# Performance work log

Measured on AMD Instinct MI355X. Metric: run time of the kernel, lower is better.

Reference implementation:

```python
import jax, jax.numpy as jnp
import numpy as np


def setup_inputs() -> dict:
    key = jax.random.key(0)
    ks = jax.random.split(key, 6)
    B, L, F, C, H, D1 = 262144, 20, 7, 16, 16, 8
    s = 0.1
    return {
        "x": jax.random.normal(ks[0], (B, L, F), dtype=jnp.float32),
        "conv_w": jax.random.normal(ks[1], (3, F, C), dtype=jnp.float32) * s,
        "conv_b": jnp.zeros((C,), dtype=jnp.float32),
        "rnn_w": jax.random.normal(ks[2], (C, H), dtype=jnp.float32) * s,
        "rnn_u": jax.random.normal(ks[3], (H, H), dtype=jnp.float32) * s,
        "rnn_b": jnp.zeros((H,), dtype=jnp.float32),
        "d1_w": jax.random.normal(ks[4], (H, D1), dtype=jnp.float32) * s,
        "d1_b": jnp.zeros((D1,), dtype=jnp.float32),
        "out_w": jax.random.normal(ks[5], (D1, 1), dtype=jnp.float32) * s,
        "out_b": jnp.zeros((1,), dtype=jnp.float32),
    }


def reference(x, conv_w, conv_b, rnn_w, rnn_u, rnn_b, d1_w, d1_b, out_w, out_b):
    # Conv1D, kernel 3, 'same' padding, relu.  x: [B,L,F] -> [B,L,C]
    h = jax.lax.conv_general_dilated(
        x, conv_w, window_strides=(1,), padding="SAME",
        dimension_numbers=("NWC", "WIO", "NWC"))
    h = jax.nn.relu(h + conv_b)

    # SimpleRNN(16), tanh, return last state.  Precompute input projections.
    xw = jnp.einsum("blc,ch->blh", h, rnn_w) + rnn_b  # [B,L,H]
    xw_t = jnp.swapaxes(xw, 0, 1)                      # [L,B,H]

    def step(state, xt):
        new = jnp.tanh(xt + state @ rnn_u)
        return new, None

    h0 = jnp.zeros((x.shape[0], rnn_u.shape[0]), dtype=x.dtype)
    h_last, _ = jax.lax.scan(step, h0, xw_t)           # [B,H]

    z = jax.nn.relu(h_last @ d1_w + d1_b)              # [B,8]
    return z @ out_w + out_b                           # [B,1]
```

## Files before the change

kernel.cpp:

```cpp
#include <hip/hip_runtime.h>


#define BLK 256
#define LSEQ 20
#define EPD 92
#define LOG2E2 2.8853900817779268f

typedef _Float16 f16;
typedef __fp16   fp16x2 __attribute__((ext_vector_type(2)));
typedef _Float16 f16x4 __attribute__((ext_vector_type(4)));
typedef _Float16 f16x8 __attribute__((ext_vector_type(8)));
typedef float    f32x4 __attribute__((ext_vector_type(4)));

union UB128 { uint4 q; f16x8 v; };
union UB64  { f16x4 v; fp16x2 p[2]; };
union HU    { fp16x2 p; uint u; };

__global__ __launch_bounds__(BLK, 6) void hybrid_fwd(
    const float* __restrict__ x,
    const float* __restrict__ conv_w, const float* __restrict__ conv_b,
    const float* __restrict__ rnn_w,  const float* __restrict__ rnn_u,
    const float* __restrict__ rnn_b,
    const float* __restrict__ d1_w,   const float* __restrict__ d1_b,
    const float* __restrict__ out_w,  const float* __restrict__ out_b,
    float* __restrict__ out)
{
    __shared__ __align__(16) uint xs[64 * EPD];

    const int tid  = threadIdx.x;
    const int wave = tid >> 6, lane = tid & 63;
    const int b16  = lane & 15, g = lane >> 4;
    const long BE  = (long)blockIdx.x * 64;

    #pragma unroll
    for (int k = 0; k < 3; ++k) {
        int t = tid + k * BLK;
        int e = t / 12, s = t - e * 12;
        xs[e * EPD + (s < 4 ? s : 80 + s)] = ((s & 3) == 3) ? 0x3C000000u : 0u;
    }
    const float* xg = x + BE * 140;
    #pragma unroll 2
    for (int k = 0; k < 5; ++k) {
        int t = tid + k * BLK;
        int e = t / 20, r = t - e * 20;
        const float* rp = xg + e * 140 + r * 7;
        float f0 = rp[0], f1 = rp[1], f2 = rp[2], f3 = rp[3];
        float f4 = rp[4], f5 = rp[5], f6 = rp[6];
        HU h0, h1, h2, h3;
        h0.p = __builtin_amdgcn_cvt_pkrtz(f0, f1);
        h1.p = __builtin_amdgcn_cvt_pkrtz(f2, f3);
        h2.p = __builtin_amdgcn_cvt_pkrtz(f4, f5);
        h3.p = __builtin_amdgcn_cvt_pkrtz(f6, 1.0f);
        uint4 val; val.x = h0.u; val.y = h1.u; val.z = h2.u; val.w = h3.u;
        *(uint4*)&xs[e * EPD + 4 * (r + 1)] = val;
    }
    __syncthreads();

    f16x8 A1;
    #pragma unroll
    for (int t = 0; t < 8; ++t) {
        float wv = conv_w[min(g * 7 + t, 20) * 16 + b16];
        float sel = (g < 3 && t < 7) ? wv
                  : ((g == 3 && t == 7) ? conv_b[b16] : 0.f);
        A1[t] = (f16)sel;
    }
    f16x4 A2, AU;
    f32x4 rbp;
    #pragma unroll
    for (int t = 0; t < 4; ++t) {
        A2[t]  = (f16)(LOG2E2 * rnn_w[(4 * g + t) * 16 + b16]);
        AU[t]  = (f16)(LOG2E2 * rnn_u[(4 * g + t) * 16 + b16]);
        rbp[t] = LOG2E2 * rnn_b[4 * g + t];
    }
    const f32x4 zero4 = {0.f, 0.f, 0.f, 0.f};

    const uint* rbase = xs + (wave * 16 + b16) * EPD + 4 * g;

    f16x4 H = {};

    #pragma unroll 4
    for (int l = 0; l < LSEQ; ++l) {
        UB128 B1;
        B1.q = *(const uint4*)(rbase + 4 * l);
        f32x4 a1 = __builtin_amdgcn_mfma_f32_16x16x32_f16(A1, B1.v, zero4, 0, 0, 0);
        UB64 B2;
        B2.p[0] = __builtin_amdgcn_cvt_pkrtz(fmaxf(a1[0], 0.f), fmaxf(a1[1], 0.f));
        B2.p[1] = __builtin_amdgcn_cvt_pkrtz(fmaxf(a1[2], 0.f), fmaxf(a1[3], 0.f));
        f32x4 a2 = __builtin_amdgcn_mfma_f32_16x16x16f16(A2, B2.v, rbp, 0, 0, 0);
        a2 = __builtin_amdgcn_mfma_f32_16x16x16f16(AU, H, a2, 0, 0, 0);
        float t0 = __builtin_amdgcn_rcpf(1.f + __builtin_amdgcn_exp2f(a2[0]));
        float t1 = __builtin_amdgcn_rcpf(1.f + __builtin_amdgcn_exp2f(a2[1]));
        float t2 = __builtin_amdgcn_rcpf(1.f + __builtin_amdgcn_exp2f(a2[2]));
        float t3 = __builtin_amdgcn_rcpf(1.f + __builtin_amdgcn_exp2f(a2[3]));
        UB64 Hn;
        Hn.p[0] = __builtin_amdgcn_cvt_pkrtz(fmaf(-2.f, t0, 1.f), fmaf(-2.f, t1, 1.f));
        Hn.p[1] = __builtin_amdgcn_cvt_pkrtz(fmaf(-2.f, t2, 1.f), fmaf(-2.f, t3, 1.f));
        H = Hn.v;
    }

    f16x4 A3;
    f32x4 c3;
    #pragma unroll
    for (int t = 0; t < 4; ++t) {
        int j = 4 * g + t;
        A3[t] = (f16)(b16 < 8 ? d1_w[j * 8 + b16] : 0.f);
        c3[t] = d1_b[min(j, 7)];
    }
    f32x4 a3 = __builtin_amdgcn_mfma_f32_16x16x16f16(A3, H, c3, 0, 0, 0);
    float part = 0.f;
    #pragma unroll
    for (int r = 0; r < 4; ++r) {
        int d = 4 * g + r;
        float wv = (g < 2) ? out_w[min(d, 7)] : 0.f;
        part = fmaf(fmaxf(a3[r], 0.f), wv, part);
    }
    part += __shfl_xor(part, 16);
    part += __shfl_xor(part, 32);
    if (lane < 16)
        out[BE + wave * 16 + lane] = part + out_b[0];
}

extern "C" void kernel_launch(void* const* d_in, const int* in_sizes, int n_in,
                              void* d_out, int out_size, void* d_ws, size_t ws_size,
                              hipStream_t stream) {
    const float* x      = (const float*)d_in[0];
    const float* conv_w = (const float*)d_in[1];
    const float* conv_b = (const float*)d_in[2];
    const float* rnn_w  = (const float*)d_in[3];
    const float* rnn_u  = (const float*)d_in[4];
    const float* rnn_b  = (const float*)d_in[5];
    const float* d1_w   = (const float*)d_in[6];
    const float* d1_b   = (const float*)d_in[7];
    const float* out_w  = (const float*)d_in[8];
    const float* out_b  = (const float*)d_in[9];
    float* out = (float*)d_out;

    const int B = out_size;
    const int grid = B / 64;
    hybrid_fwd<<<grid, BLK, 0, stream>>>(x, conv_w, conv_b, rnn_w, rnn_u, rnn_b,
                                         d1_w, d1_b, out_w, out_b, out);
}
```

Measured before the change: 46.99 us.

## Make blocks persistent over four tiles with double-buffered LDS prefetch

Each block now processes four 64-element tiles in sequence. While the RNN recurrence runs on the current tile, the next tile's input is prefetched into registers with coalesced float4 loads and then written into a second LDS buffer. Padding rows are set up once per buffer, weights are loaded once per block, and the grid shrinks by a factor of four. The cost is double the LDS, more registers, fewer resident blocks per CU (launch bound lowered from 6 to 3), and scattered 2-byte LDS stores in place of packed 16-byte stores.

```diff
diff --git a/kernel.cpp b/kernel.cpp
--- a/kernel.cpp
+++ b/kernel.cpp
@@ -3,7 +3,10 @@
 
 #define BLK 256
 #define LSEQ 20
-#define EPD 92
+#define EPB 64
+#define EPW 84
+#define TILE_DW (EPB*EPW + 8)
+#define NT 4
 #define LOG2E2 2.8853900817779268f
 
 typedef _Float16 f16;
@@ -14,9 +17,38 @@
 
 union UB128 { uint4 q; f16x8 v; };
 union UB64  { f16x4 v; fp16x2 p[2]; };
-union HU    { fp16x2 p; uint u; };
 
-__global__ __launch_bounds__(BLK, 6) void hybrid_fwd(
+__device__ __forceinline__ void issue_loads(const float4* __restrict__ xsrc,
+                                            int tid, float4 (&v)[9]) {
+    #pragma unroll
+    for (int k = 0; k < 9; ++k) {
+        int g4 = tid + k * BLK;
+        if (g4 < 2240) v[k] = xsrc[g4];
+    }
+}
+
+__device__ __forceinline__ void write_tile(uint* tile, int tid,
+                                           const float4 (&v)[9]) {
+    #pragma unroll
+    for (int k = 0; k < 9; ++k) {
+        int g4 = tid + k * BLK;
+        if (g4 < 2240) {
+            int e = g4 / 35, j = g4 - e * 35;
+            int p = 4 * j;
+            int r = p / 7, c = p - 7 * r;
+            char* eb = (char*)(tile + e * EPW);
+            *(f16*)(eb + (r + 1) * 16 + 2 * c) = (f16)v[k].x;
+            if (++c == 7) { c = 0; ++r; }
+            *(f16*)(eb + (r + 1) * 16 + 2 * c) = (f16)v[k].y;
+            if (++c == 7) { c = 0; ++r; }
+            *(f16*)(eb + (r + 1) * 16 + 2 * c) = (f16)v[k].z;
+            if (++c == 7) { c = 0; ++r; }
+            *(f16*)(eb + (r + 1) * 16 + 2 * c) = (f16)v[k].w;
+        }
+    }
+}
+
+__global__ __launch_bounds__(BLK, 3) void hybrid_fwd(
     const float* __restrict__ x,
     const float* __restrict__ conv_w, const float* __restrict__ conv_b,
     const float* __restrict__ rnn_w,  const float* __restrict__ rnn_u,
@@ -25,36 +57,25 @@
     const float* __restrict__ out_w,  const float* __restrict__ out_b,
     float* __restrict__ out)
 {
-    __shared__ __align__(16) uint xs[64 * EPD];
+    __shared__ __align__(16) uint xs[2][TILE_DW];
 
     const int tid  = threadIdx.x;
     const int wave = tid >> 6, lane = tid & 63;
     const int b16  = lane & 15, g = lane >> 4;
-    const long BE  = (long)blockIdx.x * 64;
+    const long blockElem = (long)blockIdx.x * (EPB * NT);
 
+    const uint4 PAD = make_uint4(0u, 0u, 0u, 0x3C000000u);
     #pragma unroll
-    for (int k = 0; k < 3; ++k) {
-        int t = tid + k * BLK;
-        int e = t / 12, s = t - e * 12;
-        xs[e * EPD + (s < 4 ? s : 80 + s)] = ((s & 3) == 3) ? 0x3C000000u : 0u;
+    for (int b = 0; b < 2; ++b) {
+        if (tid < EPB) *(uint4*)(xs[b] + tid * EPW) = PAD;
+        if (tid < 2)   *(uint4*)(xs[b] + EPB * EPW + 4 * tid) = PAD;
+        #pragma unroll
+        for (int k = 0; k < 5; ++k) {
+            int t = tid + k * BLK;
+            int e = t / 20, s = t - e * 20;
+            *(f16*)((char*)(xs[b] + e * EPW) + (s + 1) * 16 + 14) = (f16)1.0f;
+        }
     }
-    const float* xg = x + BE * 140;
-    #pragma unroll 2
-    for (int k = 0; k < 5; ++k) {
-        int t = tid + k * BLK;
-        int e = t / 20, r = t - e * 20;
-        const float* rp = xg + e * 140 + r * 7;
-        float f0 = rp[0], f1 = rp[1], f2 = rp[2], f3 = rp[3];
-        float f4 = rp[4], f5 = rp[5], f6 = rp[6];
-        HU h0, h1, h2, h3;
-        h0.p = __builtin_amdgcn_cvt_pkrtz(f0, f1);
-        h1.p = __builtin_amdgcn_cvt_pkrtz(f2, f3);
-        h2.p = __builtin_amdgcn_cvt_pkrtz(f4, f5);
-        h3.p = __builtin_amdgcn_cvt_pkrtz(f6, 1.0f);
-        uint4 val; val.x = h0.u; val.y = h1.u; val.z = h2.u; val.w = h3.u;
-        *(uint4*)&xs[e * EPD + 4 * (r + 1)] = val;
-    }
-    __syncthreads();
 
     f16x8 A1;
     #pragma unroll
@@ -72,32 +93,6 @@
         AU[t]  = (f16)(LOG2E2 * rnn_u[(4 * g + t) * 16 + b16]);
         rbp[t] = LOG2E2 * rnn_b[4 * g + t];
     }
-    const f32x4 zero4 = {0.f, 0.f, 0.f, 0.f};
-
-    const uint* rbase = xs + (wave * 16 + b16) * EPD + 4 * g;
-
-    f16x4 H = {};
-
-    #pragma unroll 4
-    for (int l = 0; l < LSEQ; ++l) {
-        UB128 B1;
-        B1.q = *(const uint4*)(rbase + 4 * l);
-        f32x4 a1 = __builtin_amdgcn_mfma_f32_16x16x32_f16(A1, B1.v, zero4, 0, 0, 0);
-        UB64 B2;
-        B2.p[0] = __builtin_amdgcn_cvt_pkrtz(fmaxf(a1[0], 0.f), fmaxf(a1[1], 0.f));
-        B2.p[1] = __builtin_amdgcn_cvt_pkrtz(fmaxf(a1[2], 0.f), fmaxf(a1[3], 0.f));
-        f32x4 a2 = __builtin_amdgcn_mfma_f32_16x16x16f16(A2, B2.v, rbp, 0, 0, 0);
-        a2 = __builtin_amdgcn_mfma_f32_16x16x16f16(AU, H, a2, 0, 0, 0);
-        float t0 = __builtin_amdgcn_rcpf(1.f + __builtin_amdgcn_exp2f(a2[0]));
-        float t1 = __builtin_amdgcn_rcpf(1.f + __builtin_amdgcn_exp2f(a2[1]));
-        float t2 = __builtin_amdgcn_rcpf(1.f + __builtin_amdgcn_exp2f(a2[2]));
-        float t3 = __builtin_amdgcn_rcpf(1.f + __builtin_amdgcn_exp2f(a2[3]));
-        UB64 Hn;
-        Hn.p[0] = __builtin_amdgcn_cvt_pkrtz(fmaf(-2.f, t0, 1.f), fmaf(-2.f, t1, 1.f));
-        Hn.p[1] = __builtin_amdgcn_cvt_pkrtz(fmaf(-2.f, t2, 1.f), fmaf(-2.f, t3, 1.f));
-        H = Hn.v;
-    }
-
     f16x4 A3;
     f32x4 c3;
     #pragma unroll
@@ -106,18 +101,59 @@
         A3[t] = (f16)(b16 < 8 ? d1_w[j * 8 + b16] : 0.f);
         c3[t] = d1_b[min(j, 7)];
     }
-    f32x4 a3 = __builtin_amdgcn_mfma_f32_16x16x16f16(A3, H, c3, 0, 0, 0);
-    float part = 0.f;
+    float ow[4];
     #pragma unroll
-    for (int r = 0; r < 4; ++r) {
-        int d = 4 * g + r;
-        float wv = (g < 2) ? out_w[min(d, 7)] : 0.f;
-        part = fmaf(fmaxf(a3[r], 0.f), wv, part);
+    for (int r = 0; r < 4; ++r)
+        ow[r] = (g < 2) ? out_w[min(4 * g + r, 7)] : 0.f;
+    const float ob = out_b[0];
+    const f32x4 zero4 = {0.f, 0.f, 0.f, 0.f};
+
+    float4 v[9];
+    issue_loads((const float4*)(x + blockElem * 140), tid, v);
+    write_tile(xs[0], tid, v);
+    __syncthreads();
+
+    #pragma unroll
+    for (int t = 0; t < NT; ++t) {
+        if (t < NT - 1)
+            issue_loads((const float4*)(x + (blockElem + (t + 1) * EPB) * 140), tid, v);
+
+        const uint* rb0 = xs[t & 1] + (wave * 16 + b16) * EPW + 4 * g;
+        f16x4 H = {};
+        #pragma unroll
+        for (int l = 0; l < LSEQ; ++l) {
+            UB128 B1;
+            B1.q = *(const uint4*)(rb0 + 4 * l);
+            f32x4 a1 = __builtin_amdgcn_mfma_f32_16x16x32_f16(A1, B1.v, zero4, 0, 0, 0);
+            UB64 B2;
+            B2.p[0] = __builtin_amdgcn_cvt_pkrtz(fmaxf(a1[0], 0.f), fmaxf(a1[1], 0.f));
+            B2.p[1] = __builtin_amdgcn_cvt_pkrtz(fmaxf(a1[2], 0.f), fmaxf(a1[3], 0.f));
+            f32x4 a2 = __builtin_amdgcn_mfma_f32_16x16x16f16(A2, B2.v, rbp, 0, 0, 0);
+            a2 = __builtin_amdgcn_mfma_f32_16x16x16f16(AU, H, a2, 0, 0, 0);
+            float t0 = __builtin_amdgcn_rcpf(1.f + __builtin_amdgcn_exp2f(a2[0]));
+            float t1 = __builtin_amdgcn_rcpf(1.f + __builtin_amdgcn_exp2f(a2[1]));
+            float t2 = __builtin_amdgcn_rcpf(1.f + __builtin_amdgcn_exp2f(a2[2]));
+            float t3 = __builtin_amdgcn_rcpf(1.f + __builtin_amdgcn_exp2f(a2[3]));
+            UB64 Hn;
+            Hn.p[0] = __builtin_amdgcn_cvt_pkrtz(fmaf(-2.f, t0, 1.f), fmaf(-2.f, t1, 1.f));
+            Hn.p[1] = __builtin_amdgcn_cvt_pkrtz(fmaf(-2.f, t2, 1.f), fmaf(-2.f, t3, 1.f));
+            H = Hn.v;
+        }
+        f32x4 a3 = __builtin_amdgcn_mfma_f32_16x16x16f16(A3, H, c3, 0, 0, 0);
+        float part = 0.f;
+        #pragma unroll
+        for (int r = 0; r < 4; ++r)
+            part = fmaf(fmaxf(a3[r], 0.f), ow[r], part);
+        part += __shfl_xor(part, 16);
+        part += __shfl_xor(part, 32);
+        if (lane < 16)
+            out[blockElem + t * EPB + wave * 16 + b16] = part + ob;
+
+        if (t < NT - 1) {
+            write_tile(xs[(t + 1) & 1], tid, v);
+            __syncthreads();
+        }
     }
-    part += __shfl_xor(part, 16);
-    part += __shfl_xor(part, 32);
-    if (lane < 16)
-        out[BE + wave * 16 + lane] = part + out_b[0];
 }
 
 extern "C" void kernel_launch(void* const* d_in, const int* in_sizes, int n_in,
@@ -136,7 +172,7 @@
     float* out = (float*)d_out;
 
     const int B = out_size;
-    const int grid = B / 64;
+    const int grid = B / (EPB * NT);
     hybrid_fwd<<<grid, BLK, 0, stream>>>(x, conv_w, conv_b, rnn_w, rnn_u, rnn_b,
                                          d1_w, d1_b, out_w, out_b, out);
 }
```

New measurement: 45.37 us. 1.04x faster.

## Interleave four independent RNN chains per wave and load each sequence per thread

Applied to the files above, without the earlier changes.

Each wave now processes 64 sequences as four interleaved 16-sequence MFMA chains, so the serial recurrence latency of one chain is hidden behind the others. The block shrinks to 128 threads handling 128 sequences, with one thread loading a whole sequence as float4 vectors into shared memory using a tighter row pitch. This cuts the number of blocks and removes the per-element index division in the load. In exchange it raises register pressure, lowers the launch-bounds occupancy hint, and turns global reads into per-thread strided accesses, which may coalesce poorly.

```diff
diff --git a/kernel.cpp b/kernel.cpp
--- a/kernel.cpp
+++ b/kernel.cpp
@@ -1,9 +1,10 @@
 #include <hip/hip_runtime.h>
 
 
-#define BLK 256
+#define BLK 128
 #define LSEQ 20
-#define EPD 92
+#define EPB 128
+#define EPW 84
 #define LOG2E2 2.8853900817779268f
 
 typedef _Float16 f16;
@@ -16,7 +17,7 @@
 union UB64  { f16x4 v; fp16x2 p[2]; };
 union HU    { fp16x2 p; uint u; };
 
-__global__ __launch_bounds__(BLK, 6) void hybrid_fwd(
+__global__ __launch_bounds__(BLK, 2) void hybrid_fwd(
     const float* __restrict__ x,
     const float* __restrict__ conv_w, const float* __restrict__ conv_b,
     const float* __restrict__ rnn_w,  const float* __restrict__ rnn_u,
@@ -25,36 +26,38 @@
     const float* __restrict__ out_w,  const float* __restrict__ out_b,
     float* __restrict__ out)
 {
-    __shared__ __align__(16) uint xs[64 * EPD];
+    __shared__ __align__(16) uint xs[EPB * EPW + 8];
 
     const int tid  = threadIdx.x;
     const int wave = tid >> 6, lane = tid & 63;
     const int b16  = lane & 15, g = lane >> 4;
-    const long BE  = (long)blockIdx.x * 64;
+    const long BE  = (long)blockIdx.x * EPB;
 
-    #pragma unroll
-    for (int k = 0; k < 3; ++k) {
-        int t = tid + k * BLK;
-        int e = t / 12, s = t - e * 12;
-        xs[e * EPD + (s < 4 ? s : 80 + s)] = ((s & 3) == 3) ? 0x3C000000u : 0u;
+    const uint4 PAD = make_uint4(0u, 0u, 0u, 0x3C000000u);
+    *(uint4*)(xs + tid * EPW) = PAD;
+    if (tid < 2) *(uint4*)(xs + EPB * EPW + 4 * tid) = PAD;
+
+    {
+        const float4* src = (const float4*)(x + (BE + tid) * 140);
+        uint* eb = xs + tid * EPW;
+        #pragma unroll
+        for (int k = 0; k < 5; ++k) {
+            float4 v[7];
+            #pragma unroll
+            for (int j = 0; j < 7; ++j) v[j] = src[7 * k + j];
+            const float* f = (const float*)v;
+            #pragma unroll
+            for (int i = 0; i < 4; ++i) {
+                HU h0, h1, h2, h3;
+                h0.p = __builtin_amdgcn_cvt_pkrtz(f[7 * i + 0], f[7 * i + 1]);
+                h1.p = __builtin_amdgcn_cvt_pkrtz(f[7 * i + 2], f[7 * i + 3]);
+                h2.p = __builtin_amdgcn_cvt_pkrtz(f[7 * i + 4], f[7 * i + 5]);
+                h3.p = __builtin_amdgcn_cvt_pkrtz(f[7 * i + 6], 1.0f);
+                uint4 val; val.x = h0.u; val.y = h1.u; val.z = h2.u; val.w = h3.u;
+                *(uint4*)(eb + 4 * (4 * k + i + 1)) = val;
+            }
+        }
     }
-    const float* xg = x + BE * 140;
-    #pragma unroll 2
-    for (int k = 0; k < 5; ++k) {
-        int t = tid + k * BLK;
-        int e = t / 20, r = t - e * 20;
-        const float* rp = xg + e * 140 + r * 7;
-        float f0 = rp[0], f1 = rp[1], f2 = rp[2], f3 = rp[3];
-        float f4 = rp[4], f5 = rp[5], f6 = rp[6];
-        HU h0, h1, h2, h3;
-        h0.p = __builtin_amdgcn_cvt_pkrtz(f0, f1);
-        h1.p = __builtin_amdgcn_cvt_pkrtz(f2, f3);
-        h2.p = __builtin_amdgcn_cvt_pkrtz(f4, f5);
-        h3.p = __builtin_amdgcn_cvt_pkrtz(f6, 1.0f);
-        uint4 val; val.x = h0.u; val.y = h1.u; val.z = h2.u; val.w = h3.u;
-        *(uint4*)&xs[e * EPD + 4 * (r + 1)] = val;
-    }
-    __syncthreads();
 
     f16x8 A1;
     #pragma unroll
@@ -72,32 +75,6 @@
         AU[t]  = (f16)(LOG2E2 * rnn_u[(4 * g + t) * 16 + b16]);
         rbp[t] = LOG2E2 * rnn_b[4 * g + t];
     }
-    const f32x4 zero4 = {0.f, 0.f, 0.f, 0.f};
-
-    const uint* rbase = xs + (wave * 16 + b16) * EPD + 4 * g;
-
-    f16x4 H = {};
-
-    #pragma unroll 4
-    for (int l = 0; l < LSEQ; ++l) {
-        UB128 B1;
-        B1.q = *(const uint4*)(rbase + 4 * l);
-        f32x4 a1 = __builtin_amdgcn_mfma_f32_16x16x32_f16(A1, B1.v, zero4, 0, 0, 0);
-        UB64 B2;
-        B2.p[0] = __builtin_amdgcn_cvt_pkrtz(fmaxf(a1[0], 0.f), fmaxf(a1[1], 0.f));
-        B2.p[1] = __builtin_amdgcn_cvt_pkrtz(fmaxf(a1[2], 0.f), fmaxf(a1[3], 0.f));
-        f32x4 a2 = __builtin_amdgcn_mfma_f32_16x16x16f16(A2, B2.v, rbp, 0, 0, 0);
-        a2 = __builtin_amdgcn_mfma_f32_16x16x16f16(AU, H, a2, 0, 0, 0);
-        float t0 = __builtin_amdgcn_rcpf(1.f + __builtin_amdgcn_exp2f(a2[0]));
-        float t1 = __builtin_amdgcn_rcpf(1.f + __builtin_amdgcn_exp2f(a2[1]));
-        float t2 = __builtin_amdgcn_rcpf(1.f + __builtin_amdgcn_exp2f(a2[2]));
-        float t3 = __builtin_amdgcn_rcpf(1.f + __builtin_amdgcn_exp2f(a2[3]));
-        UB64 Hn;
-        Hn.p[0] = __builtin_amdgcn_cvt_pkrtz(fmaf(-2.f, t0, 1.f), fmaf(-2.f, t1, 1.f));
-        Hn.p[1] = __builtin_amdgcn_cvt_pkrtz(fmaf(-2.f, t2, 1.f), fmaf(-2.f, t3, 1.f));
-        H = Hn.v;
-    }
-
     f16x4 A3;
     f32x4 c3;
     #pragma unroll
@@ -106,18 +83,58 @@
         A3[t] = (f16)(b16 < 8 ? d1_w[j * 8 + b16] : 0.f);
         c3[t] = d1_b[min(j, 7)];
     }
-    f32x4 a3 = __builtin_amdgcn_mfma_f32_16x16x16f16(A3, H, c3, 0, 0, 0);
-    float part = 0.f;
+    float ow[4];
     #pragma unroll
-    for (int r = 0; r < 4; ++r) {
-        int d = 4 * g + r;
-        float wv = (g < 2) ? out_w[min(d, 7)] : 0.f;
-        part = fmaf(fmaxf(a3[r], 0.f), wv, part);
+    for (int r = 0; r < 4; ++r)
+        ow[r] = (g < 2) ? out_w[min(4 * g + r, 7)] : 0.f;
+    const float ob = out_b[0];
+    const f32x4 zero4 = {0.f, 0.f, 0.f, 0.f};
+
+    __syncthreads();
+
+    const uint* rbase = xs + ((wave << 6) + b16) * EPW + 4 * g;
+
+    f16x4 H[4] = {{}, {}, {}, {}};
+    #pragma unroll
+    for (int l = 0; l < LSEQ; ++l) {
+        #pragma unroll
+        for (int c = 0; c < 4; ++c) {
+            UB128 B1;
+            B1.q = *(const uint4*)(rbase + c * 16 * EPW + 4 * l);
+            f32x4 a1 = __builtin_amdgcn_mfma_f32_16x16x32_f16(A1, B1.v, zero4, 0, 0, 0);
+            UB64 B2;
+            B2.p[0] = __builtin_amdgcn_cvt_pkrtz(fmaxf(a1[0], 0.f), fmaxf(a1[1], 0.f));
+            B2.p[1] = __builtin_amdgcn_cvt_pkrtz(fmaxf(a1[2], 0.f), fmaxf(a1[3], 0.f));
+            f32x4 a2 = __builtin_amdgcn_mfma_f32_16x16x16f16(A2, B2.v, rbp, 0, 0, 0);
+            a2 = __builtin_amdgcn_mfma_f32_16x16x16f16(AU, H[c], a2, 0, 0, 0);
+            float t0 = __builtin_amdgcn_rcpf(1.f + __builtin_amdgcn_exp2f(a2[0]));
+            float t1 = __builtin_amdgcn_rcpf(1.f + __builtin_amdgcn_exp2f(a2[1]));
+            float t2 = __builtin_amdgcn_rcpf(1.f + __builtin_amdgcn_exp2f(a2[2]));
+            float t3 = __builtin_amdgcn_rcpf(1.f + __builtin_amdgcn_exp2f(a2[3]));
+            UB64 Hn;
+            Hn.p[0] = __builtin_amdgcn_cvt_pkrtz(fmaf(-2.f, t0, 1.f), fmaf(-2.f, t1, 1.f));
+            Hn.p[1] = __builtin_amdgcn_cvt_pkrtz(fmaf(-2.f, t2, 1.f), fmaf(-2.f, t3, 1.f));
+            H[c] = Hn.v;
+        }
     }
-    part += __shfl_xor(part, 16);
-    part += __shfl_xor(part, 32);
-    if (lane < 16)
-        out[BE + wave * 16 + lane] = part + out_b[0];
+
+    float p[4];
+    #pragma unroll
+    for (int c = 0; c < 4; ++c) {
+        f32x4 a3 = __builtin_amdgcn_mfma_f32_16x16x16f16(A3, H[c], c3, 0, 0, 0);
+        float part = 0.f;
+        #pragma unroll
+        for (int r = 0; r < 4; ++r)
+            part = fmaf(fmaxf(a3[r], 0.f), ow[r], part);
+        part += __shfl_xor(part, 16);
+        part += __shfl_xor(part, 32);
+        p[c] = part;
+    }
+    if (lane < 16) {
+        #pragma unroll
+        for (int c = 0; c < 4; ++c)
+            out[BE + (wave << 6) + c * 16 + b16] = p[c] + ob;
+    }
 }
 
 extern "C" void kernel_launch(void* const* d_in, const int* in_sizes, int n_in,
@@ -136,7 +153,7 @@
     float* out = (float*)d_out;
 
     const int B = out_size;
-    const int grid = B / 64;
+    const int grid = B / EPB;
     hybrid_fwd<<<grid, BLK, 0, stream>>>(x, conv_w, conv_b, rnn_w, rnn_u, rnn_b,
                                          d1_w, d1_b, out_w, out_b, out);
 }
```

Result: slower. 62.08 us (+32.1%).

## Make LDS staging wave-private, drop block barrier and pad rows, shrink block

Applied to the files above, without the earlier changes.

Each wave now stages its own 16 sequences into a private LDS region, so the block-wide __syncthreads is replaced by a local lgkmcnt wait and the zero and one padding slots are removed. The conv boundary handling moves into the weights: at the first and last timestep, zeroed A1 variants and redirected load addresses stand in for the missing neighbours. Global loads become two overlapping float4 reads per row, and the block shrinks to 128 threads with a higher occupancy hint. The cost is more register pressure from the extra weight variants and hoisted epilogue parameters, plus possibly unaligned or out-of-range float4 reads on the last row.

```diff
diff --git a/kernel.cpp b/kernel.cpp
--- a/kernel.cpp
+++ b/kernel.cpp
@@ -1,9 +1,10 @@
 #include <hip/hip_runtime.h>
 
 
-#define BLK 256
+#define BLK 128
 #define LSEQ 20
-#define EPD 92
+#define EPW 80
+#define WREG (16*EPW)
 #define LOG2E2 2.8853900817779268f
 
 typedef _Float16 f16;
@@ -16,7 +17,7 @@
 union UB64  { f16x4 v; fp16x2 p[2]; };
 union HU    { fp16x2 p; uint u; };
 
-__global__ __launch_bounds__(BLK, 6) void hybrid_fwd(
+__global__ __launch_bounds__(BLK, 8) void hybrid_fwd(
     const float* __restrict__ x,
     const float* __restrict__ conv_w, const float* __restrict__ conv_b,
     const float* __restrict__ rnn_w,  const float* __restrict__ rnn_u,
@@ -25,36 +26,13 @@
     const float* __restrict__ out_w,  const float* __restrict__ out_b,
     float* __restrict__ out)
 {
-    __shared__ __align__(16) uint xs[64 * EPD];
+    __shared__ __align__(16) uint xs[2 * WREG];
 
     const int tid  = threadIdx.x;
     const int wave = tid >> 6, lane = tid & 63;
     const int b16  = lane & 15, g = lane >> 4;
-    const long BE  = (long)blockIdx.x * 64;
-
-    #pragma unroll
-    for (int k = 0; k < 3; ++k) {
-        int t = tid + k * BLK;
-        int e = t / 12, s = t - e * 12;
-        xs[e * EPD + (s < 4 ? s : 80 + s)] = ((s & 3) == 3) ? 0x3C000000u : 0u;
-    }
-    const float* xg = x + BE * 140;
-    #pragma unroll 2
-    for (int k = 0; k < 5; ++k) {
-        int t = tid + k * BLK;
-        int e = t / 20, r = t - e * 20;
-        const float* rp = xg + e * 140 + r * 7;
-        float f0 = rp[0], f1 = rp[1], f2 = rp[2], f3 = rp[3];
-        float f4 = rp[4], f5 = rp[5], f6 = rp[6];
-        HU h0, h1, h2, h3;
-        h0.p = __builtin_amdgcn_cvt_pkrtz(f0, f1);
-        h1.p = __builtin_amdgcn_cvt_pkrtz(f2, f3);
-        h2.p = __builtin_amdgcn_cvt_pkrtz(f4, f5);
-        h3.p = __builtin_amdgcn_cvt_pkrtz(f6, 1.0f);
-        uint4 val; val.x = h0.u; val.y = h1.u; val.z = h2.u; val.w = h3.u;
-        *(uint4*)&xs[e * EPD + 4 * (r + 1)] = val;
-    }
-    __syncthreads();
+    const long BE  = (long)blockIdx.x * 32;
+    uint* wb = xs + wave * WREG;
 
     f16x8 A1;
     #pragma unroll
@@ -64,6 +42,9 @@
                   : ((g == 3 && t == 7) ? conv_b[b16] : 0.f);
         A1[t] = (f16)sel;
     }
+    const f16x8 A1z = {};
+    const f16x8 A1_0  = (g == 0) ? A1z : A1;
+    const f16x8 A1_19 = (g == 2) ? A1z : A1;
     f16x4 A2, AU;
     f32x4 rbp;
     #pragma unroll
@@ -72,17 +53,57 @@
         AU[t]  = (f16)(LOG2E2 * rnn_u[(4 * g + t) * 16 + b16]);
         rbp[t] = LOG2E2 * rnn_b[4 * g + t];
     }
+    f16x4 A3;
+    f32x4 c3;
+    #pragma unroll
+    for (int t = 0; t < 4; ++t) {
+        int j = 4 * g + t;
+        A3[t] = (f16)(b16 < 8 ? d1_w[j * 8 + b16] : 0.f);
+        c3[t] = d1_b[min(j, 7)];
+    }
+    float ow[4];
+    #pragma unroll
+    for (int r = 0; r < 4; ++r)
+        ow[r] = (g < 2) ? out_w[min(4 * g + r, 7)] : 0.f;
+    const float ob = out_b[0];
     const f32x4 zero4 = {0.f, 0.f, 0.f, 0.f};
 
-    const uint* rbase = xs + (wave * 16 + b16) * EPD + 4 * g;
+    {
+        const float* xg = x + (BE + wave * 16) * 140;
+        #pragma unroll
+        for (int k = 0; k < 5; ++k) {
+            int rowflat = lane + 64 * k;
+            int e = rowflat / 20;
+            int r = rowflat - e * 20;
+            const float* rp = xg + e * 140 + r * 7;
+            float4 v0 = *(const float4*)(rp);
+            float4 v1 = *(const float4*)(rp + 3);
+            HU h0, h1, h2, h3;
+            h0.p = __builtin_amdgcn_cvt_pkrtz(v0.x, v0.y);
+            h1.p = __builtin_amdgcn_cvt_pkrtz(v0.z, v0.w);
+            h2.p = __builtin_amdgcn_cvt_pkrtz(v1.y, v1.z);
+            h3.p = __builtin_amdgcn_cvt_pkrtz(v1.w, 1.0f);
+            uint4 val; val.x = h0.u; val.y = h1.u; val.z = h2.u; val.w = h3.u;
+            *(uint4*)(wb + e * EPW + 4 * r) = val;
+        }
+    }
+
+    asm volatile("s_waitcnt lgkmcnt(0)" ::: "memory");
+    __builtin_amdgcn_sched_barrier(0);
+
+    const int d = (g == 3) ? 0 : (g - 1);
+    const uint* p0 = wb + b16 * EPW + 4 * d;
+    const uint* a0   = (b16 == 0  && g == 0) ? wb : p0;
+    const uint* aL19 = (b16 == 15 && g == 2) ? wb : (p0 + 76);
 
     f16x4 H = {};
-
-    #pragma unroll 4
+    #pragma unroll
     for (int l = 0; l < LSEQ; ++l) {
+        const f16x8 Al = (l == 0) ? A1_0 : (l == LSEQ - 1) ? A1_19 : A1;
+        const uint* aL = (l == 0) ? a0 : (l == LSEQ - 1) ? aL19 : (p0 + 4 * l);
         UB128 B1;
-        B1.q = *(const uint4*)(rbase + 4 * l);
-        f32x4 a1 = __builtin_amdgcn_mfma_f32_16x16x32_f16(A1, B1.v, zero4, 0, 0, 0);
+        B1.q = *(const uint4*)aL;
+        f32x4 a1 = __builtin_amdgcn_mfma_f32_16x16x32_f16(Al, B1.v, zero4, 0, 0, 0);
         UB64 B2;
         B2.p[0] = __builtin_amdgcn_cvt_pkrtz(fmaxf(a1[0], 0.f), fmaxf(a1[1], 0.f));
         B2.p[1] = __builtin_amdgcn_cvt_pkrtz(fmaxf(a1[2], 0.f), fmaxf(a1[3], 0.f));
@@ -98,26 +119,15 @@
         H = Hn.v;
     }
 
-    f16x4 A3;
-    f32x4 c3;
-    #pragma unroll
-    for (int t = 0; t < 4; ++t) {
-        int j = 4 * g + t;
-        A3[t] = (f16)(b16 < 8 ? d1_w[j * 8 + b16] : 0.f);
-        c3[t] = d1_b[min(j, 7)];
-    }
     f32x4 a3 = __builtin_amdgcn_mfma_f32_16x16x16f16(A3, H, c3, 0, 0, 0);
     float part = 0.f;
     #pragma unroll
-    for (int r = 0; r < 4; ++r) {
-        int d = 4 * g + r;
-        float wv = (g < 2) ? out_w[min(d, 7)] : 0.f;
-        part = fmaf(fmaxf(a3[r], 0.f), wv, part);
-    }
+    for (int r = 0; r < 4; ++r)
+        part = fmaf(fmaxf(a3[r], 0.f), ow[r], part);
     part += __shfl_xor(part, 16);
     part += __shfl_xor(part, 32);
     if (lane < 16)
-        out[BE + wave * 16 + lane] = part + out_b[0];
+        out[BE + wave * 16 + b16] = part + ob;
 }
 
 extern "C" void kernel_launch(void* const* d_in, const int* in_sizes, int n_in,
@@ -136,7 +146,7 @@
     float* out = (float*)d_out;
 
     const int B = out_size;
-    const int grid = B / 64;
+    const int grid = B / 32;
     hybrid_fwd<<<grid, BLK, 0, stream>>>(x, conv_w, conv_b, rnn_w, rnn_u, rnn_b,
                                          d1_w, d1_b, out_w, out_b, out);
 }
```

After: 42.30 us. 10.0% less time.
